# Kernel optimization log

Hardware: AMD Instinct MI355X
Metric: run time of the kernel (lower is better)

The kernel has to match this reference:

```python
import jax, jax.numpy as jnp
import numpy as np

D, H, K, L, F, G, M, OUT = 1280, 16, 80, 4, 5120, 48, 2, 2048
HALF = K // 2  # rotary half dim = 40


def _token_coords(grid_thw, merge_size, N):
    tpi = grid_thw[:, 0] * grid_thw[:, 1] * grid_thw[:, 2]
    cu = jnp.concatenate([jnp.zeros(1, jnp.int32), jnp.cumsum(tpi).astype(jnp.int32)])
    tok = jnp.arange(N, dtype=jnp.int32)
    img_id = jnp.searchsorted(cu[1:], tok, side='right')
    local = tok - cu[img_id]
    h = grid_thw[img_id, 1]
    w = grid_thw[img_id, 2]
    spatial = local % (h * w)
    msq = merge_size * merge_size
    mw = w // merge_size
    group, intra = spatial // msq, spatial % msq
    row = (group // mw) * merge_size + intra // merge_size
    col = (group % mw) * merge_size + intra % merge_size
    return row, col, h, w, cu


def _layernorm(x, s, b, eps=1e-6):
    mu = jnp.mean(x, -1, keepdims=True)
    var = jnp.mean(jnp.square(x - mu), -1, keepdims=True)
    return (x - mu) * jax.lax.rsqrt(var + eps) * s + b


def _rotate_half(x):
    x1, x2 = x[..., :HALF], x[..., HALF:]
    return jnp.concatenate([-x2, x1], axis=-1)


def setup_inputs() -> dict:
    key = jax.random.key(0)
    ks = jax.random.split(key, 16)
    s = 0.02
    inp = {
        'pixels': jax.random.normal(ks[0], (2048, 1536), jnp.float32),
        'grid_thw': jnp.array([[1, 16, 32]] * 4, jnp.int32),
        'pos_embed': jax.random.normal(ks[1], (G * G, D), jnp.float32) * s,
        'patch_w': jax.random.normal(ks[2], (1536, D), jnp.float32) * s,
        'patch_b': jnp.zeros((D,), jnp.float32),
        'ln1_s': jnp.ones((L, D), jnp.float32), 'ln1_b': jnp.zeros((L, D), jnp.float32),
        'qkv_w': jax.random.normal(ks[3], (L, D, 3 * D), jnp.float32) * s,
        'qkv_b': jnp.zeros((L, 3 * D), jnp.float32),
        'proj_w': jax.random.normal(ks[4], (L, D, D), jnp.float32) * s,
        'proj_b': jnp.zeros((L, D), jnp.float32),
        'ln2_s': jnp.ones((L, D), jnp.float32), 'ln2_b': jnp.zeros((L, D), jnp.float32),
        'fc1_w': jax.random.normal(ks[5], (L, D, F), jnp.float32) * s,
        'fc1_b': jnp.zeros((L, F), jnp.float32),
        'fc2_w': jax.random.normal(ks[6], (L, F, D), jnp.float32) * s,
        'fc2_b': jnp.zeros((L, D), jnp.float32),
        'm_norm_s': jnp.ones((D,), jnp.float32), 'm_norm_b': jnp.zeros((D,), jnp.float32),
        'm_fc1_w': jax.random.normal(ks[7], (D * M * M, D * M * M), jnp.float32) * s,
        'm_fc1_b': jnp.zeros((D * M * M,), jnp.float32),
        'm_fc2_w': jax.random.normal(ks[8], (D * M * M, OUT), jnp.float32) * s,
        'm_fc2_b': jnp.zeros((OUT,), jnp.float32),
    }
    return inp


def _forward(pixels, grid_thw, pos_embed, patch_w, patch_b, ln1_s, ln1_b, qkv_w, qkv_b,
             proj_w, proj_b, ln2_s, ln2_b, fc1_w, fc1_b, fc2_w, fc2_b,
             m_norm_s, m_norm_b, m_fc1_w, m_fc1_b, m_fc2_w, m_fc2_b):
    N = pixels.shape[0]
    row, col, h, w, cu = _token_coords(grid_thw, M, N)

    # patch embed: conv with stride==kernel over flattened patches == linear
    x = pixels @ patch_w + patch_b  # [N, D]

    # bilinear position-embedding interpolation onto each image's (h, w) grid
    rf = jnp.where(h > 1, row.astype(jnp.float32) * (G - 1) / jnp.maximum(h - 1, 1), 0.0)
    cf = jnp.where(w > 1, col.astype(jnp.float32) * (G - 1) / jnp.maximum(w - 1, 1), 0.0)
    r0 = jnp.floor(rf).astype(jnp.int32); r1 = jnp.minimum(r0 + 1, G - 1)
    c0 = jnp.floor(cf).astype(jnp.int32); c1 = jnp.minimum(c0 + 1, G - 1)
    wr = (rf - r0)[:, None]; wc = (cf - c0)[:, None]
    pe = (pos_embed[r0 * G + c0] * (1 - wr) * (1 - wc)
          + pos_embed[r0 * G + c1] * (1 - wr) * wc
          + pos_embed[r1 * G + c0] * wr * (1 - wc)
          + pos_embed[r1 * G + c1] * wr * wc)
    x = x + pe

    # 2-D rotary embeddings
    inv_freq = 1.0 / (10000.0 ** (jnp.arange(0, HALF, 2, dtype=jnp.float32) / HALF))
    freqs = jnp.concatenate([row[:, None].astype(jnp.float32) * inv_freq,
                             col[:, None].astype(jnp.float32) * inv_freq], axis=-1)  # [N, HALF]
    emb = jnp.concatenate([freqs, freqs], axis=-1)  # [N, K]
    cos, sin = jnp.cos(emb)[:, None, :], jnp.sin(emb)[:, None, :]  # [N,1,K]

    # block-diagonal segment mask via cu_seqlens (N is a multiple of 128; no pad)
    tok = jnp.arange(N)
    seg = jnp.searchsorted(cu[1:], tok, side='right')
    k_start = cu[jnp.minimum(seg, cu.shape[0] - 2)]
    k_end = cu[jnp.minimum(seg + 1, cu.shape[0] - 1)]
    mask = (tok[None, :] >= k_start[:, None]) & (tok[None, :] < k_end[:, None])  # [N,N]
    scale = K ** -0.5

    for l in range(L):
        hdn = _layernorm(x, ln1_s[l], ln1_b[l])
        qkv = (hdn @ qkv_w[l] + qkv_b[l]).reshape(N, 3, H, K)
        q, k, v = qkv[:, 0], qkv[:, 1], qkv[:, 2]
        q = q * cos + _rotate_half(q) * sin
        k = k * cos + _rotate_half(k) * sin
        scores = jnp.einsum('nhk,mhk->hnm', q, k) * scale
        scores = jnp.where(mask[None], scores, jnp.finfo(scores.dtype).min)
        attn = jax.nn.softmax(scores, axis=-1)
        o = jnp.einsum('hnm,mhk->nhk', attn, v).reshape(N, D)
        x = x + o @ proj_w[l] + proj_b[l]

        hdn = _layernorm(x, ln2_s[l], ln2_b[l])
        ff = jax.nn.gelu(hdn @ fc1_w[l] + fc1_b[l], approximate=True)
        x = x + ff @ fc2_w[l] + fc2_b[l]

    # patch merger
    normed = _layernorm(x, m_norm_s, m_norm_b).reshape(N // (M * M), D * M * M)
    ff = jax.nn.gelu(normed @ m_fc1_w + m_fc1_b, approximate=True)
    return ff @ m_fc2_w + m_fc2_b  # [N/4, OUT]


def reference(pixels, grid_thw, pos_embed, patch_w, patch_b, ln1_s, ln1_b, qkv_w, qkv_b,
              proj_w, proj_b, ln2_s, ln2_b, fc1_w, fc1_b, fc2_w, fc2_b,
              m_norm_s, m_norm_b, m_fc1_w, m_fc1_b, m_fc2_w, m_fc2_b):
    return _forward(pixels, grid_thw, pos_embed, patch_w, patch_b, ln1_s, ln1_b, qkv_w, qkv_b,
                    proj_w, proj_b, ln2_s, ln2_b, fc1_w, fc1_b, fc2_w, fc2_b,
                    m_norm_s, m_norm_b, m_fc1_w, m_fc1_b, m_fc2_w, m_fc2_b)
```

## Files before the change

### kernel.cpp

```cpp
#include <hip/hip_runtime.h>
#include <math.h>

#define DMODEL 1280
#define NHEADS 16
#define FDIM   5120
#define GPOS   48
#define SEG    512

typedef __attribute__((ext_vector_type(8))) short bf16x8;
typedef __attribute__((ext_vector_type(4))) float f32x4;
typedef unsigned short u16;

__device__ __forceinline__ u16 f2bf(float f) {
  unsigned int u = __float_as_uint(f);
  u = (u + 0x7FFFu + ((u >> 16) & 1u)) >> 16;
  return (u16)u;
}
__device__ __forceinline__ float bf2f(u16 u) {
  return __uint_as_float((unsigned int)u << 16);
}
__device__ __forceinline__ float gelu_tanh(float x) {
  float u = 0.7978845608028654f * (x + 0.044715f * x * x * x);
  float t = __expf(2.f * u);
  float th = 1.f - 2.f / (t + 1.f);
  return 0.5f * x * (1.f + th);
}

typedef const __attribute__((address_space(1))) unsigned int* gas_t;
typedef __attribute__((address_space(3))) unsigned int* las_t;
__device__ __forceinline__ void async16(const void* g, void* l) {
  __builtin_amdgcn_global_load_lds((gas_t)g, (las_t)l, 16, 0, 0);
}

__device__ __forceinline__ int xcd_remap(int b, int nwg) {
  int q = nwg >> 3, r = nwg & 7, x = b & 7, d = b >> 3;
  return (x < r ? x * (q + 1) : r * (q + 1) + (x - r) * q) + d;
}

#define STG256(mat, PW, ldx, h, kk, pp)                          \
  do {                                                           \
    const u16* g_ = (PW) + (long long)(h) * 128 * (ldx) + (kk);  \
    async16(g_, &L[pp][mat][h][(w * 2 + 0) * 512]);              \
    async16(g_ + 32, &L[pp][mat][h][(w * 2 + 1) * 512]);         \
  } while (0)

#define MM256(ii, ff)                                                          \
  acc[ii][ff] = __builtin_amdgcn_mfma_f32_16x16x32_bf16(aR[(ii) & 3][0],       \
                    bR[ff][0], acc[ii][ff], 0, 0, 0);                          \
  acc[ii][ff] = __builtin_amdgcn_mfma_f32_16x16x32_bf16(aR[(ii) & 3][1],       \
                    bR[ff][1], acc[ii][ff], 0, 0, 0);

#define BAR256() asm volatile("s_barrier" ::: "memory")
#define LGKM0() asm volatile("s_waitcnt lgkmcnt(0)" ::: "memory")

template <int EPI>
__global__ __launch_bounds__(512, 2) void gemm256(
    const u16* __restrict__ A, const u16* __restrict__ B,
    const float* __restrict__ bias, void* __restrict__ Cv,
    int Kd, int lda, int ldb, int ldc, int nsplit, long long pstride) {
  __shared__ __align__(16) u16 L[2][2][2][8192];
  const int sp = blockIdx.z;
  const int Ks = Kd / nsplit;
  const int NT = Ks >> 6;
  const u16* Ab = A + (long long)sp * Ks;
  const u16* Bb = B + (long long)sp * Ks;
  const int gx = gridDim.x;
  const int lg = xcd_remap(blockIdx.x + gx * blockIdx.y, gx * gridDim.y);
  const int m0 = (lg % gx) * 256, n0 = (lg / gx) * 256;
  const int t = threadIdx.x, ln = t & 63, w = t >> 6;
  const int wr = w >> 2, wc = w & 3;
  const int m16 = ln & 15, q = ln >> 4;
  const int r16 = ln >> 2;
  const int csw = (ln & 3) ^ ((ln >> 5) << 1);
  const int rbase = m16 * 32 + (q ^ ((m16 >> 3) << 1)) * 8;

  const u16* Aw = Ab + (long long)(m0 + w * 16 + r16) * lda + csw * 8;
  const u16* Bw = Bb + (long long)(n0 + w * 16 + r16) * ldb + csw * 8;

  f32x4 acc[8][4];
#pragma unroll
  for (int i = 0; i < 8; i++)
#pragma unroll
    for (int j = 0; j < 4; j++)
#pragma unroll
      for (int r = 0; r < 4; r++) acc[i][j][r] = 0.f;

  STG256(0, Aw, lda, 0, 0, 0);
  STG256(0, Aw, lda, 1, 0, 0);
  STG256(1, Bw, ldb, 0, 0, 0);
  STG256(1, Bw, ldb, 1, 0, 0);
  if (NT > 1) {
    STG256(1, Bw, ldb, 0, 64, 1);
    STG256(1, Bw, ldb, 1, 64, 1);
    asm volatile("s_waitcnt vmcnt(4)" ::: "memory");
  } else {
    asm volatile("s_waitcnt vmcnt(0)" ::: "memory");
  }
  BAR256();

  const int wb = (wc & 1) * 4;
  for (int tt = 0; tt < NT; ++tt) {
    const int p = tt & 1;
    const u16* Abuf = &L[p][0][wr][0];
    const u16* Bbuf = &L[p][1][wc >> 1][0];
    bf16x8 aR[4][2], bR[4][2];

#pragma unroll
    for (int i = 0; i < 4; ++i) {
      aR[i][0] = *(const bf16x8*)(Abuf + (i * 2 + 0) * 512 + rbase);
      aR[i][1] = *(const bf16x8*)(Abuf + (i * 2 + 1) * 512 + rbase);
    }
#pragma unroll
    for (int fc = 0; fc < 2; ++fc) {
      bR[fc][0] = *(const bf16x8*)(Bbuf + ((wb + fc) * 2 + 0) * 512 + rbase);
      bR[fc][1] = *(const bf16x8*)(Bbuf + ((wb + fc) * 2 + 1) * 512 + rbase);
    }
    if (tt + 1 < NT) STG256(0, Aw, lda, 0, (tt + 1) * 64, (tt + 1) & 1);
    BAR256();
    LGKM0();
    __builtin_amdgcn_s_setprio(1);
#pragma unroll
    for (int i = 0; i < 4; ++i) { MM256(i, 0); MM256(i, 1); }
    __builtin_amdgcn_s_setprio(0);
    BAR256();

#pragma unroll
    for (int fc = 2; fc < 4; ++fc) {
      bR[fc][0] = *(const bf16x8*)(Bbuf + ((wb + fc) * 2 + 0) * 512 + rbase);
      bR[fc][1] = *(const bf16x8*)(Bbuf + ((wb + fc) * 2 + 1) * 512 + rbase);
    }
    if (tt + 1 < NT) STG256(0, Aw, lda, 1, (tt + 1) * 64, (tt + 1) & 1);
    BAR256();
    LGKM0();
    __builtin_amdgcn_s_setprio(1);
#pragma unroll
    for (int i = 0; i < 4; ++i) { MM256(i, 2); MM256(i, 3); }
    __builtin_amdgcn_s_setprio(0);
    BAR256();

#pragma unroll
    for (int i = 0; i < 4; ++i) {
      aR[i][0] = *(const bf16x8*)(Abuf + ((4 + i) * 2 + 0) * 512 + rbase);
      aR[i][1] = *(const bf16x8*)(Abuf + ((4 + i) * 2 + 1) * 512 + rbase);
    }
    if (tt + 2 < NT) STG256(1, Bw, ldb, 0, (tt + 2) * 64, p);
    BAR256();
    LGKM0();
    __builtin_amdgcn_s_setprio(1);
#pragma unroll
    for (int i = 0; i < 4; ++i) { MM256(4 + i, 2); MM256(4 + i, 3); }
    __builtin_amdgcn_s_setprio(0);
    BAR256();

    if (tt + 2 < NT) STG256(1, Bw, ldb, 1, (tt + 2) * 64, p);
    BAR256();
    LGKM0();
    __builtin_amdgcn_s_setprio(1);
#pragma unroll
    for (int i = 0; i < 4; ++i) { MM256(4 + i, 0); MM256(4 + i, 1); }
    __builtin_amdgcn_s_setprio(0);
    if (tt + 1 < NT) {
      if (tt + 2 < NT) asm volatile("s_waitcnt vmcnt(4)" ::: "memory");
      else             asm volatile("s_waitcnt vmcnt(0)" ::: "memory");
    }
    BAR256();
  }

#pragma unroll
  for (int fr = 0; fr < 8; fr++) {
#pragma unroll
    for (int r = 0; r < 4; r++) {
      int row = m0 + wr * 128 + fr * 16 + q * 4 + r;
      if (EPI == 0) {
        u16* Cp = (u16*)Cv + (long long)sp * pstride + (long long)row * ldc;
#pragma unroll
        for (int fc = 0; fc < 4; fc++)
          Cp[n0 + wc * 64 + fc * 16 + m16] = f2bf(acc[fr][fc][r]);
      } else if (EPI == 1) {
        u16* Cb = (u16*)Cv + (long long)row * ldc;
#pragma unroll
        for (int fc = 0; fc < 4; fc++) {
          int col = n0 + wc * 64 + fc * 16 + m16;
          Cb[col] = f2bf(acc[fr][fc][r] + bias[col]);
        }
      } else {
        u16* Cb = (u16*)Cv + (long long)row * ldc;
#pragma unroll
        for (int fc = 0; fc < 4; fc++) {
          int col = n0 + wc * 64 + fc * 16 + m16;
          Cb[col] = f2bf(gelu_tanh(acc[fr][fc][r] + bias[col]));
        }
      }
    }
  }
}

__global__ __launch_bounds__(256) void fattn_k(
    const u16* __restrict__ qr, const u16* __restrict__ kr,
    const u16* __restrict__ vpT, u16* __restrict__ o, int N, float iscale) {
  __shared__ __align__(16) u16 Ks[2][24][512];
  __shared__ __align__(16) u16 Vs[2][20][512];
  __shared__ __align__(16) u16 Ps[4][32 * 128];
  const int nseg = N >> 9;
  const int gx = gridDim.x;
  const int lg = xcd_remap(blockIdx.x + gx * blockIdx.y, gx * gridDim.y);
  const int strip = lg % gx, hb = lg / gx;
  const int h = hb / nseg, seg = hb - h * nseg;
  const int t = threadIdx.x, ln = t & 63, w = t >> 6;
  const int m16 = ln & 15, qh = ln >> 4;
  const int r4 = ln >> 2, gsw = (ln & 3) ^ ((ln >> 5) << 1);
  const int rbase = m16 * 32 + ((qh ^ ((m16 >> 3) << 1)) << 3);
  const long long hN = (long long)h * N;
  const int segbase = seg * SEG;
  const int q0 = segbase + strip * 128 + w * 32;

  bf16x8 qf[2][3];
#pragma unroll
  for (int mi = 0; mi < 2; mi++)
#pragma unroll
    for (int ks = 0; ks < 3; ks++)
      qf[mi][ks] = *(const bf16x8*)&qr[(hN + q0 + mi * 16 + m16) * 96 + ks * 32 + qh * 8];

  f32x4 ao[2][5];
#pragma unroll
  for (int mi = 0; mi < 2; mi++)
#pragma unroll
    for (int df = 0; df < 5; df++)
#pragma unroll
      for (int r = 0; r < 4; r++) ao[mi][df][r] = 0.f;
  float m_[2][4], l_[2][4];
#pragma unroll
  for (int mi = 0; mi < 2; mi++)
#pragma unroll
    for (int r = 0; r < 4; r++) { m_[mi][r] = -1e30f; l_[mi][r] = 0.f; }

  auto stage = [&](int c, int pb) {
#pragma unroll
    for (int i = 0; i < 6; i++) {
      int sK = w * 6 + i, f = sK / 3, kg = sK - f * 3;
      async16(&kr[(hN + segbase + c * 128 + f * 16 + r4) * 96 + kg * 32 + gsw * 8],
              &Ks[pb][sK][0]);
    }
#pragma unroll
    for (int i = 0; i < 5; i++) {
      int sV = w * 5 + i, df = sV >> 2, kvg = sV & 3;
      async16(&vpT[((long long)hb * 128 + df * 16 + r4) * SEG + c * 128 + kvg * 32 + gsw * 8],
              &Vs[pb][sV][0]);
    }
  };

  stage(0, 0);
  u16* Pmy = &Ps[w][0];
  for (int c = 0; c < 4; c++) {
    const int pb = c & 1;
    __syncthreads();
    if (c < 3) stage(c + 1, pb ^ 1);

    f32x4 s[2][8];
#pragma unroll
    for (int mi = 0; mi < 2; mi++)
#pragma unroll
      for (int f = 0; f < 8; f++)
#pragma unroll
        for (int r = 0; r < 4; r++) s[mi][f][r] = 0.f;
#pragma unroll
    for (int ks = 0; ks < 3; ks++) {
#pragma unroll
      for (int f = 0; f < 8; f++) {
        bf16x8 kf = *(const bf16x8*)&Ks[pb][f * 3 + ks][rbase];
#pragma unroll
        for (int mi = 0; mi < 2; mi++)
          s[mi][f] = __builtin_amdgcn_mfma_f32_16x16x32_bf16(qf[mi][ks], kf, s[mi][f], 0, 0, 0);
      }
    }

#pragma unroll
    for (int mi = 0; mi < 2; mi++) {
#pragma unroll
      for (int r = 0; r < 4; r++) {
        float mx = s[mi][0][r];
#pragma unroll
        for (int f = 1; f < 8; f++) mx = fmaxf(mx, s[mi][f][r]);
        mx *= iscale;
#pragma unroll
        for (int o2 = 1; o2 <= 8; o2 <<= 1) mx = fmaxf(mx, __shfl_xor(mx, o2));
        float mn = fmaxf(m_[mi][r], mx);
        float corr = __expf(m_[mi][r] - mn);
        m_[mi][r] = mn;
        float rs = 0.f;
#pragma unroll
        for (int f = 0; f < 8; f++) {
          float p = __expf(s[mi][f][r] * iscale - mn);
          s[mi][f][r] = p;
          rs += p;
        }
#pragma unroll
        for (int o2 = 1; o2 <= 8; o2 <<= 1) rs += __shfl_xor(rs, o2);
        l_[mi][r] = l_[mi][r] * corr + rs;
#pragma unroll
        for (int df = 0; df < 5; df++) ao[mi][df][r] *= corr;
      }
    }

#pragma unroll
    for (int mi = 0; mi < 2; mi++) {
#pragma unroll
      for (int r = 0; r < 4; r++) {
        int qq = mi * 16 + qh * 4 + r;
        int base = qq * 128 + (m16 & 7);
        int ql = qq & 7;
#pragma unroll
        for (int f = 0; f < 8; f++) {
          int gr = (f * 2 + (m16 >> 3)) ^ ql;
          Pmy[base + gr * 8] = f2bf(s[mi][f][r]);
        }
      }
    }

#pragma unroll
    for (int ks = 0; ks < 4; ks++) {
      bf16x8 pf[2];
#pragma unroll
      for (int mi = 0; mi < 2; mi++)
        pf[mi] = *(const bf16x8*)&Pmy[(mi * 16 + m16) * 128 +
                                      (((ks * 4 + qh) ^ (m16 & 7)) << 3)];
#pragma unroll
      for (int df = 0; df < 5; df++) {
        bf16x8 vf = *(const bf16x8*)&Vs[pb][df * 4 + ks][rbase];
#pragma unroll
        for (int mi = 0; mi < 2; mi++)
          ao[mi][df] = __builtin_amdgcn_mfma_f32_16x16x32_bf16(pf[mi], vf, ao[mi][df], 0, 0, 0);
      }
    }
  }

#pragma unroll
  for (int mi = 0; mi < 2; mi++) {
#pragma unroll
    for (int r = 0; r < 4; r++) {
      float rl = 1.f / l_[mi][r];
      long long rowb = (long long)(q0 + mi * 16 + qh * 4 + r) * DMODEL + h * 80;
#pragma unroll
      for (int df = 0; df < 5; df++)
        o[rowb + df * 16 + m16] = f2bf(ao[mi][df][r] * rl);
    }
  }
}

template <int S, int RES, int GELU, int OUTBF>
__global__ void reduce_k(const u16* __restrict__ Pp, long long mn, int Nn,
                         const float* __restrict__ bias,
                         const float* __restrict__ res, void* __restrict__ out) {
  long long i = ((long long)blockIdx.x * 256 + threadIdx.x) * 4;
  if (i >= mn) return;
  float vx = 0.f, vy = 0.f, vz = 0.f, vw = 0.f;
#pragma unroll
  for (int s = 0; s < S; s++) {
    ushort4 u4 = *(const ushort4*)(Pp + (long long)s * mn + i);
    vx += bf2f(u4.x); vy += bf2f(u4.y); vz += bf2f(u4.z); vw += bf2f(u4.w);
  }
  int col = (int)(i % Nn);
  vx += bias[col]; vy += bias[col + 1]; vz += bias[col + 2]; vw += bias[col + 3];
  if (GELU) {
    vx = gelu_tanh(vx); vy = gelu_tanh(vy);
    vz = gelu_tanh(vz); vw = gelu_tanh(vw);
  }
  if (RES) {
    float4 r4 = *(const float4*)(res + i);
    vx += r4.x; vy += r4.y; vz += r4.z; vw += r4.w;
  }
  if (OUTBF) {
    ushort4 o; o.x = f2bf(vx); o.y = f2bf(vy); o.z = f2bf(vz); o.w = f2bf(vw);
    *(ushort4*)((u16*)out + i) = o;
  } else {
    float4 o; o.x = vx; o.y = vy; o.z = vz; o.w = vw;
    *(float4*)((float*)out + i) = o;
  }
}

template <int S>
__global__ void redln_k(const u16* __restrict__ Pp, long long mn,
                        const float* __restrict__ bias,
                        float* __restrict__ x,
                        const float* __restrict__ s, const float* __restrict__ b,
                        u16* __restrict__ h) {
  int row = blockIdx.x;
  int d = threadIdx.x * 4;
  long long base = (long long)row * DMODEL + d;
  float vx = 0.f, vy = 0.f, vz = 0.f, vw = 0.f;
#pragma unroll
  for (int si = 0; si < S; si++) {
    ushort4 u4 = *(const ushort4*)(Pp + (long long)si * mn + base);
    vx += bf2f(u4.x); vy += bf2f(u4.y); vz += bf2f(u4.z); vw += bf2f(u4.w);
  }
  vx += bias[d]; vy += bias[d + 1]; vz += bias[d + 2]; vw += bias[d + 3];
  float4 r4 = *(const float4*)(x + base);
  vx += r4.x; vy += r4.y; vz += r4.z; vw += r4.w;
  float4 xv; xv.x = vx; xv.y = vy; xv.z = vz; xv.w = vw;
  *(float4*)(x + base) = xv;
  float sum = vx + vy + vz + vw;
#pragma unroll
  for (int o = 32; o; o >>= 1) sum += __shfl_xor(sum, o);
  __shared__ float red[8];
  int wv = threadIdx.x >> 6, lnn = threadIdx.x & 63;
  if (lnn == 0) red[wv] = sum;
  __syncthreads();
  float mu = 0.f;
  for (int i = 0; i < 5; i++) mu += red[i];
  mu *= (1.f / DMODEL);
  float dx = vx - mu, dy = vy - mu, dz = vz - mu, dw = vw - mu;
  float s2 = dx * dx + dy * dy + dz * dz + dw * dw;
#pragma unroll
  for (int o = 32; o; o >>= 1) s2 += __shfl_xor(s2, o);
  __syncthreads();
  if (lnn == 0) red[wv] = s2;
  __syncthreads();
  float var = 0.f;
  for (int i = 0; i < 5; i++) var += red[i];
  var *= (1.f / DMODEL);
  float rs = rsqrtf(var + 1e-6f);
  ushort4 o4;
  o4.x = f2bf(dx * rs * s[d] + b[d]);
  o4.y = f2bf(dy * rs * s[d + 1] + b[d + 1]);
  o4.z = f2bf(dz * rs * s[d + 2] + b[d + 2]);
  o4.w = f2bf(dw * rs * s[d + 3] + b[d + 3]);
  *(ushort4*)(h + base) = o4;
}

__global__ void wconv_k(const float* __restrict__ in, u16* __restrict__ out,
                        int K, int N) {
  __shared__ float tl[32][33];
  int n0 = blockIdx.x * 32, k0 = blockIdx.y * 32;
  int t = threadIdx.x;
  int r = t >> 5, c = t & 31;
#pragma unroll
  for (int i = 0; i < 4; i++)
    tl[r + 8 * i][c] = in[(long long)(k0 + r + 8 * i) * N + n0 + c];
  __syncthreads();
  int n = t >> 4, kp = (t & 15) * 2;
#pragma unroll
  for (int i = 0; i < 2; i++) {
    ushort2 o;
    o.x = f2bf(tl[kp][n + 16 * i]);
    o.y = f2bf(tl[kp + 1][n + 16 * i]);
    *(ushort2*)&out[(long long)(n0 + n + 16 * i) * K + k0 + kp] = o;
  }
}

__global__ void conv_k(const float* __restrict__ in, u16* __restrict__ out,
                       long long n) {
  long long i = ((long long)blockIdx.x * 256 + threadIdx.x) * 4;
  if (i >= n) return;
  float4 v = *(const float4*)(in + i);
  ushort4 o; o.x = f2bf(v.x); o.y = f2bf(v.y); o.z = f2bf(v.z); o.w = f2bf(v.w);
  *(ushort4*)&out[i] = o;
}

union U16x8 { uint4 v; u16 s[8]; };
__global__ void vtr_k(const u16* __restrict__ in, u16* __restrict__ out) {
  __shared__ u16 tl[64][65];
  int b = blockIdx.z;
  int m0 = blockIdx.x * 64;
  int d0 = blockIdx.y * 64;
  const u16* ib = in + (long long)b * SEG * 128;
  u16* ob = out + (long long)b * 128 * SEG;
  int t = threadIdx.x;
  int r = t >> 3, c8 = (t & 7) * 8;
#pragma unroll
  for (int i = 0; i < 2; i++) {
    U16x8 ld;
    ld.v = *(const uint4*)&ib[(long long)(m0 + r + 32 * i) * 128 + d0 + c8];
#pragma unroll
    for (int j = 0; j < 8; j++) tl[r + 32 * i][c8 + j] = ld.s[j];
  }
  __syncthreads();
  int d = t >> 3, m8 = (t & 7) * 8;
#pragma unroll
  for (int i = 0; i < 2; i++) {
    int dd = d + 32 * i;
    U16x8 st;
#pragma unroll
    for (int j = 0; j < 8; j++) st.s[j] = tl[m8 + j][dd];
    *(uint4*)&ob[(long long)(d0 + dd) * SEG + m0 + m8] = st.v;
  }
}

__global__ void coords_k(const int* __restrict__ g, int nimg,
                         int* __restrict__ rw, int* __restrict__ cl,
                         int* __restrict__ hh, int* __restrict__ ww, int N) {
  int t = blockIdx.x * 256 + threadIdx.x;
  if (t >= N) return;
  int c = 0, local = 0, H = 1, W = 1;
  for (int i = 0; i < nimg; i++) {
    int tpi = g[i * 3] * g[i * 3 + 1] * g[i * 3 + 2];
    if (t >= c && t < c + tpi) { local = t - c; H = g[i * 3 + 1]; W = g[i * 3 + 2]; }
    c += tpi;
  }
  int hw = H * W;
  int sp = local % hw;
  int mw = W >> 1;
  int gr = sp >> 2, intra = sp & 3;
  rw[t] = (gr / mw) * 2 + (intra >> 1);
  cl[t] = (gr % mw) * 2 + (intra & 1);
  hh[t] = H; ww[t] = W;
}

__global__ void peadd_k(float* __restrict__ x, const float* __restrict__ pe,
                        const int* __restrict__ rw, const int* __restrict__ cl,
                        const int* __restrict__ hh, const int* __restrict__ ww) {
  int n = blockIdx.x;
  int d = threadIdx.x * 4;
  int H = hh[n], W = ww[n];
  float rf = (H > 1) ? (float)rw[n] * (float)(GPOS - 1) / (float)(H - 1) : 0.f;
  float cf = (W > 1) ? (float)cl[n] * (float)(GPOS - 1) / (float)(W - 1) : 0.f;
  int r0 = (int)floorf(rf), c0 = (int)floorf(cf);
  int r1 = min(r0 + 1, GPOS - 1), c1 = min(c0 + 1, GPOS - 1);
  float wr = rf - (float)r0, wc = cf - (float)c0;
  float w00 = (1.f - wr) * (1.f - wc), w01 = (1.f - wr) * wc;
  float w10 = wr * (1.f - wc), w11 = wr * wc;
  float4 v00 = *(const float4*)(pe + (long long)(r0 * GPOS + c0) * DMODEL + d);
  float4 v01 = *(const float4*)(pe + (long long)(r0 * GPOS + c1) * DMODEL + d);
  float4 v10 = *(const float4*)(pe + (long long)(r1 * GPOS + c0) * DMODEL + d);
  float4 v11 = *(const float4*)(pe + (long long)(r1 * GPOS + c1) * DMODEL + d);
  float4 xv = *(float4*)(x + (long long)n * DMODEL + d);
  xv.x += w00 * v00.x + w01 * v01.x + w10 * v10.x + w11 * v11.x;
  xv.y += w00 * v00.y + w01 * v01.y + w10 * v10.y + w11 * v11.y;
  xv.z += w00 * v00.z + w01 * v01.z + w10 * v10.z + w11 * v11.z;
  xv.w += w00 * v00.w + w01 * v01.w + w10 * v10.w + w11 * v11.w;
  *(float4*)(x + (long long)n * DMODEL + d) = xv;
}

__global__ void ln_k(const float* __restrict__ X, u16* __restrict__ Y,
                     const float* __restrict__ s, const float* __restrict__ b) {
  int row = blockIdx.x;
  int d = threadIdx.x * 4;
  const float* x = X + (long long)row * DMODEL;
  float4 v = *(const float4*)(x + d);
  float sum = v.x + v.y + v.z + v.w;
#pragma unroll
  for (int o = 32; o; o >>= 1) sum += __shfl_xor(sum, o);
  __shared__ float red[8];
  int wv = threadIdx.x >> 6, lnn = threadIdx.x & 63;
  if (lnn == 0) red[wv] = sum;
  __syncthreads();
  float mu = 0.f;
  for (int i = 0; i < 5; i++) mu += red[i];
  mu *= (1.f / DMODEL);
  float dx = v.x - mu, dy = v.y - mu, dz = v.z - mu, dw = v.w - mu;
  float s2 = dx * dx + dy * dy + dz * dz + dw * dw;
#pragma unroll
  for (int o = 32; o; o >>= 1) s2 += __shfl_xor(s2, o);
  __syncthreads();
  if (lnn == 0) red[wv] = s2;
  __syncthreads();
  float var = 0.f;
  for (int i = 0; i < 5; i++) var += red[i];
  var *= (1.f / DMODEL);
  float rs = rsqrtf(var + 1e-6f);
  ushort4 o4;
  o4.x = f2bf(dx * rs * s[d] + b[d]);
  o4.y = f2bf(dy * rs * s[d + 1] + b[d + 1]);
  o4.z = f2bf(dz * rs * s[d + 2] + b[d + 2]);
  o4.w = f2bf(dw * rs * s[d + 3] + b[d + 3]);
  *(ushort4*)(Y + (long long)row * DMODEL + d) = o4;
}

__global__ void rope_k(const u16* __restrict__ qkv, const int* __restrict__ rw,
                       const int* __restrict__ cl, u16* __restrict__ qr,
                       u16* __restrict__ kr, u16* __restrict__ vp, int N) {
  int n = blockIdx.x, h = blockIdx.y, t = threadIdx.x;
  const u16* src = qkv + (long long)n * (3 * DMODEL) + h * 80;
  long long ob96 = ((long long)h * N + n) * 96;
  long long ob128 = ((long long)h * N + n) * 128;
  if (t < 40) {
    float pos = (t < 20) ? (float)rw[n] : (float)cl[n];
    float infr = exp2f(-13.287712379549449f * (float)(t % 20) * 0.05f);
    float f = pos * infr;
    float cs = cosf(f), sn = sinf(f);
    float q0 = bf2f(src[t]), q1 = bf2f(src[t + 40]);
    qr[ob96 + t] = f2bf(q0 * cs - q1 * sn);
    qr[ob96 + t + 40] = f2bf(q1 * cs + q0 * sn);
    float k0 = bf2f(src[DMODEL + t]), k1 = bf2f(src[DMODEL + t + 40]);
    kr[ob96 + t] = f2bf(k0 * cs - k1 * sn);
    kr[ob96 + t + 40] = f2bf(k1 * cs + k0 * sn);
    vp[ob128 + t] = src[2 * DMODEL + t];
    vp[ob128 + t + 40] = src[2 * DMODEL + t + 40];
  } else {
    int u = t - 40;
    if (u < 16) { qr[ob96 + 80 + u] = 0; kr[ob96 + 80 + u] = 0; }
    vp[ob128 + 80 + u] = 0;
    vp[ob128 + 104 + u] = 0;
  }
}

static void gemm_big(hipStream_t st, int epi, const u16* A, const u16* B,
                     const float* bias, void* C, int M, int Nn, int Kd,
                     int lda, int ldb, int ldc, int nsplit) {
  dim3 g(M / 256, Nn / 256, nsplit), blk(512);
  long long ps = (long long)M * Nn;
  switch (epi) {
    case 0: gemm256<0><<<g, blk, 0, st>>>(A, B, bias, C, Kd, lda, ldb, ldc, nsplit, ps); break;
    case 1: gemm256<1><<<g, blk, 0, st>>>(A, B, bias, C, Kd, lda, ldb, ldc, nsplit, ps); break;
    default: gemm256<3><<<g, blk, 0, st>>>(A, B, bias, C, Kd, lda, ldb, ldc, nsplit, ps); break;
  }
}

extern "C" void kernel_launch(void* const* d_in, const int* in_sizes, int n_in,
                              void* d_out, int out_size, void* d_ws, size_t ws_size,
                              hipStream_t stream) {
  const float* pixels = (const float*)d_in[0];
  const int* grid_thw = (const int*)d_in[1];
  const float* pos_embed = (const float*)d_in[2];
  const float* patch_w = (const float*)d_in[3];
  const float* patch_b = (const float*)d_in[4];
  const float* ln1_s = (const float*)d_in[5];
  const float* ln1_b = (const float*)d_in[6];
  const float* qkv_w = (const float*)d_in[7];
  const float* qkv_b = (const float*)d_in[8];
  const float* proj_w = (const float*)d_in[9];
  const float* proj_b = (const float*)d_in[10];
  const float* ln2_s = (const float*)d_in[11];
  const float* ln2_b = (const float*)d_in[12];
  const float* fc1_w = (const float*)d_in[13];
  const float* fc1_b = (const float*)d_in[14];
  const float* fc2_w = (const float*)d_in[15];
  const float* fc2_b = (const float*)d_in[16];
  const float* mns = (const float*)d_in[17];
  const float* mnb = (const float*)d_in[18];
  const float* mf1w = (const float*)d_in[19];
  const float* mf1b = (const float*)d_in[20];
  const float* mf2w = (const float*)d_in[21];
  const float* mf2b = (const float*)d_in[22];
  float* out = (float*)d_out;

  const int N = in_sizes[0] / 1536;
  const int nimg = in_sizes[1] / 3;
  const int nseg = N / SEG;
  const int nb = NHEADS * nseg;

  char* w = (char*)d_ws;
  size_t off = 0;
  auto alloc = [&](size_t bytes) -> void* {
    void* p = w + off;
    off += (bytes + 255) & ~(size_t)255;
    return p;
  };
  int* rw = (int*)alloc((size_t)N * 4);
  int* cl = (int*)alloc((size_t)N * 4);
  int* hh = (int*)alloc((size_t)N * 4);
  int* ww = (int*)alloc((size_t)N * 4);
  float* x = (float*)alloc((size_t)N * DMODEL * 4);
  u16* h = (u16*)alloc((size_t)N * DMODEL * 2);
  u16* pixbf = (u16*)alloc((size_t)N * 1536 * 2);
  u16* patchT = (u16*)alloc((size_t)DMODEL * 1536 * 2);
  u16* qkvT = (u16*)alloc((size_t)3 * DMODEL * DMODEL * 2);
  u16* projT = (u16*)alloc((size_t)DMODEL * DMODEL * 2);
  u16* fc1T = (u16*)alloc((size_t)FDIM * DMODEL * 2);
  u16* fc2T = (u16*)alloc((size_t)DMODEL * FDIM * 2);
  u16* qkvb = (u16*)alloc((size_t)N * 3 * DMODEL * 2);
  u16* qr = (u16*)alloc((size_t)NHEADS * N * 96 * 2);
  u16* kr = (u16*)alloc((size_t)NHEADS * N * 96 * 2);
  u16* vp = (u16*)alloc((size_t)NHEADS * N * 128 * 2);
  u16* vpT = (u16*)alloc((size_t)NHEADS * N * 128 * 2);
  u16* pad0 = (u16*)alloc((size_t)nb * 2 * SEG * 128 * 2);
  u16* o = (u16*)alloc((size_t)N * DMODEL * 2);
  float* bigA = (float*)alloc((size_t)nb * SEG * SEG * 4);
  float* bigB = (float*)alloc((size_t)nb * SEG * SEG * 2);
  (void)ws_size; (void)pad0;
  u16* mfc1T = qkvb;
  u16* mfc2T = pixbf;
  u16* ffb = (u16*)bigA;
  u16* mf = (u16*)bigA;
  u16* part = (u16*)bigB;

  const float iscale = 0.11180339887498949f;
  const long long mnD = (long long)N * DMODEL;

  coords_k<<<dim3((N + 255) / 256), 256, 0, stream>>>(grid_thw, nimg, rw, cl, hh, ww, N);
  conv_k<<<dim3((int)(((long long)N * 1536 / 4 + 255) / 256)), 256, 0, stream>>>(
      pixels, pixbf, (long long)N * 1536);
  wconv_k<<<dim3(DMODEL / 32, 1536 / 32), 256, 0, stream>>>(patch_w, patchT, 1536, DMODEL);
  gemm_big(stream, 0, pixbf, patchT, nullptr, part, N, DMODEL, 1536, 1536, 1536,
           DMODEL, 4);
  reduce_k<4, 0, 0, 0><<<dim3((int)((mnD / 4 + 255) / 256)), 256, 0, stream>>>(
      part, mnD, DMODEL, patch_b, nullptr, x);
  peadd_k<<<dim3(N), 320, 0, stream>>>(x, pos_embed, rw, cl, hh, ww);
  ln_k<<<dim3(N), 320, 0, stream>>>(x, h, ln1_s, ln1_b);

  for (int l = 0; l < 4; l++) {
    wconv_k<<<dim3(3 * DMODEL / 32, DMODEL / 32), 256, 0, stream>>>(
        qkv_w + (size_t)l * DMODEL * 3 * DMODEL, qkvT, DMODEL, 3 * DMODEL);
    wconv_k<<<dim3(DMODEL / 32, DMODEL / 32), 256, 0, stream>>>(
        proj_w + (size_t)l * DMODEL * DMODEL, projT, DMODEL, DMODEL);
    wconv_k<<<dim3(FDIM / 32, DMODEL / 32), 256, 0, stream>>>(
        fc1_w + (size_t)l * DMODEL * FDIM, fc1T, DMODEL, FDIM);
    wconv_k<<<dim3(DMODEL / 32, FDIM / 32), 256, 0, stream>>>(
        fc2_w + (size_t)l * FDIM * DMODEL, fc2T, FDIM, DMODEL);

    gemm_big(stream, 1, h, qkvT, qkv_b + (size_t)l * 3 * DMODEL, qkvb, N,
             3 * DMODEL, DMODEL, DMODEL, DMODEL, 3 * DMODEL, 1);
    rope_k<<<dim3(N, NHEADS), 64, 0, stream>>>(qkvb, rw, cl, qr, kr, vp, N);
    vtr_k<<<dim3(8, 2, nb), 256, 0, stream>>>(vp, vpT);
    fattn_k<<<dim3(SEG / 128, nb), 256, 0, stream>>>(qr, kr, vpT, o, N, iscale);
    gemm_big(stream, 0, o, projT, nullptr, part, N, DMODEL, DMODEL, DMODEL,
             DMODEL, DMODEL, 4);
    redln_k<4><<<dim3(N), 320, 0, stream>>>(part, mnD, proj_b + (size_t)l * DMODEL,
                                            x, ln2_s + (size_t)l * DMODEL,
                                            ln2_b + (size_t)l * DMODEL, h);
    gemm_big(stream, 3, h, fc1T, fc1_b + (size_t)l * FDIM, ffb, N, FDIM, DMODEL,
             DMODEL, DMODEL, FDIM, 1);
    gemm_big(stream, 0, ffb, fc2T, nullptr, part, N, DMODEL, FDIM, FDIM, FDIM,
             DMODEL, 4);
    const float* nsl = (l < 3) ? ln1_s + (size_t)(l + 1) * DMODEL : mns;
    const float* nbl = (l < 3) ? ln1_b + (size_t)(l + 1) * DMODEL : mnb;
    redln_k<4><<<dim3(N), 320, 0, stream>>>(part, mnD, fc2_b + (size_t)l * DMODEL,
                                            x, nsl, nbl, h);
  }

  const int Mm = N / 4;
  wconv_k<<<dim3(FDIM / 32, FDIM / 32), 256, 0, stream>>>(mf1w, mfc1T, FDIM, FDIM);
  gemm_big(stream, 0, h, mfc1T, nullptr, part, Mm, FDIM, FDIM, FDIM, FDIM, FDIM, 4);
  reduce_k<4, 0, 1, 1><<<dim3((int)(((long long)Mm * FDIM / 4 + 255) / 256)), 256, 0, stream>>>(
      part, (long long)Mm * FDIM, FDIM, mf1b, nullptr, mf);
  wconv_k<<<dim3(2048 / 32, FDIM / 32), 256, 0, stream>>>(mf2w, mfc2T, FDIM, 2048);
  gemm_big(stream, 0, mf, mfc2T, nullptr, part, Mm, 2048, FDIM, FDIM, FDIM, 2048, 16);
  reduce_k<16, 0, 0, 0><<<dim3((int)(((long long)Mm * 2048 / 4 + 255) / 256)), 256, 0, stream>>>(
      part, (long long)Mm * 2048, 2048, mf2b, nullptr, out);
}
```

Baseline: 1.441 ms.

## Shrink big GEMM tile from 256x256 to 128x128 with 4-wave blocks

Replaces the 512-thread 256x256 GEMM kernel with a 256-thread 128x128 variant. The LDS staging, fragment loads and MFMA schedule are rewritten for a 2x2 wave layout with 4x4 accumulator tiles per wave. The aim is more workgroups for the small M (2048 tokens) so more CUs are busy. The cost is less data reuse per tile and more global traffic per FLOP. It also drops the LDS wait before the last two MFMA phases, which is fine only because those phases reuse fragments already in registers.

```diff
diff --git a/kernel.cpp b/kernel.cpp
--- a/kernel.cpp
+++ b/kernel.cpp
@@ -37,28 +37,25 @@
   return (x < r ? x * (q + 1) : r * (q + 1) + (x - r) * q) + d;
 }
 
-#define STG256(mat, PW, ldx, h, kk, pp)                          \
-  do {                                                           \
-    const u16* g_ = (PW) + (long long)(h) * 128 * (ldx) + (kk);  \
-    async16(g_, &L[pp][mat][h][(w * 2 + 0) * 512]);              \
-    async16(g_ + 32, &L[pp][mat][h][(w * 2 + 1) * 512]);         \
-  } while (0)
-
-#define MM256(ii, ff)                                                          \
-  acc[ii][ff] = __builtin_amdgcn_mfma_f32_16x16x32_bf16(aR[(ii) & 3][0],       \
-                    bR[ff][0], acc[ii][ff], 0, 0, 0);                          \
-  acc[ii][ff] = __builtin_amdgcn_mfma_f32_16x16x32_bf16(aR[(ii) & 3][1],       \
+#define STG1(mat, PW, ldx, rb, kh, kk, pp)                                  \
+  async16((PW) + (long long)(rb) * 16 * (ldx) + (kk) + (kh) * 32,           \
+          &L[pp][mat][((rb) * 2 + (kh)) * 512])
+
+#define MM1(ii, ff)                                                          \
+  acc[ii][ff] = __builtin_amdgcn_mfma_f32_16x16x32_bf16(aR[ii][0],           \
+                    bR[ff][0], acc[ii][ff], 0, 0, 0);                        \
+  acc[ii][ff] = __builtin_amdgcn_mfma_f32_16x16x32_bf16(aR[ii][1],           \
                     bR[ff][1], acc[ii][ff], 0, 0, 0);
 
-#define BAR256() asm volatile("s_barrier" ::: "memory")
+#define BARX() asm volatile("s_barrier" ::: "memory")
 #define LGKM0() asm volatile("s_waitcnt lgkmcnt(0)" ::: "memory")
 
 template <int EPI>
-__global__ __launch_bounds__(512, 2) void gemm256(
+__global__ __launch_bounds__(256, 2) void gemm128(
     const u16* __restrict__ A, const u16* __restrict__ B,
     const float* __restrict__ bias, void* __restrict__ Cv,
     int Kd, int lda, int ldb, int ldc, int nsplit, long long pstride) {
-  __shared__ __align__(16) u16 L[2][2][2][8192];
+  __shared__ __align__(16) u16 L[2][2][8192];
   const int sp = blockIdx.z;
   const int Ks = Kd / nsplit;
   const int NT = Ks >> 6;
@@ -66,111 +63,109 @@
   const u16* Bb = B + (long long)sp * Ks;
   const int gx = gridDim.x;
   const int lg = xcd_remap(blockIdx.x + gx * blockIdx.y, gx * gridDim.y);
-  const int m0 = (lg % gx) * 256, n0 = (lg / gx) * 256;
+  const int m0 = (lg % gx) * 128, n0 = (lg / gx) * 128;
   const int t = threadIdx.x, ln = t & 63, w = t >> 6;
-  const int wr = w >> 2, wc = w & 3;
+  const int wr = w >> 1, wc = w & 1;
   const int m16 = ln & 15, q = ln >> 4;
   const int r16 = ln >> 2;
   const int csw = (ln & 3) ^ ((ln >> 5) << 1);
   const int rbase = m16 * 32 + (q ^ ((m16 >> 3) << 1)) * 8;
 
-  const u16* Aw = Ab + (long long)(m0 + w * 16 + r16) * lda + csw * 8;
-  const u16* Bw = Bb + (long long)(n0 + w * 16 + r16) * ldb + csw * 8;
-
-  f32x4 acc[8][4];
-#pragma unroll
-  for (int i = 0; i < 8; i++)
+  const u16* Aw = Ab + (long long)(m0 + r16) * lda + csw * 8;
+  const u16* Bw = Bb + (long long)(n0 + r16) * ldb + csw * 8;
+  const int w4 = w + 4;
+
+  f32x4 acc[4][4];
+#pragma unroll
+  for (int i = 0; i < 4; i++)
 #pragma unroll
     for (int j = 0; j < 4; j++)
 #pragma unroll
       for (int r = 0; r < 4; r++) acc[i][j][r] = 0.f;
 
-  STG256(0, Aw, lda, 0, 0, 0);
-  STG256(0, Aw, lda, 1, 0, 0);
-  STG256(1, Bw, ldb, 0, 0, 0);
-  STG256(1, Bw, ldb, 1, 0, 0);
+  STG1(0, Aw, lda, w, 0, 0, 0);  STG1(0, Aw, lda, w, 1, 0, 0);
+  STG1(0, Aw, lda, w4, 0, 0, 0); STG1(0, Aw, lda, w4, 1, 0, 0);
+  STG1(1, Bw, ldb, w, 0, 0, 0);  STG1(1, Bw, ldb, w, 1, 0, 0);
+  STG1(1, Bw, ldb, w4, 0, 0, 0); STG1(1, Bw, ldb, w4, 1, 0, 0);
   if (NT > 1) {
-    STG256(1, Bw, ldb, 0, 64, 1);
-    STG256(1, Bw, ldb, 1, 64, 1);
+    STG1(1, Bw, ldb, w, 0, 64, 1);  STG1(1, Bw, ldb, w, 1, 64, 1);
+    STG1(1, Bw, ldb, w4, 0, 64, 1); STG1(1, Bw, ldb, w4, 1, 64, 1);
     asm volatile("s_waitcnt vmcnt(4)" ::: "memory");
   } else {
     asm volatile("s_waitcnt vmcnt(0)" ::: "memory");
   }
-  BAR256();
-
-  const int wb = (wc & 1) * 4;
+  BARX();
+
   for (int tt = 0; tt < NT; ++tt) {
     const int p = tt & 1;
-    const u16* Abuf = &L[p][0][wr][0];
-    const u16* Bbuf = &L[p][1][wc >> 1][0];
+    const u16* Abuf = &L[p][0][0];
+    const u16* Bbuf = &L[p][1][0];
     bf16x8 aR[4][2], bR[4][2];
 
 #pragma unroll
     for (int i = 0; i < 4; ++i) {
-      aR[i][0] = *(const bf16x8*)(Abuf + (i * 2 + 0) * 512 + rbase);
-      aR[i][1] = *(const bf16x8*)(Abuf + (i * 2 + 1) * 512 + rbase);
-    }
-#pragma unroll
-    for (int fc = 0; fc < 2; ++fc) {
-      bR[fc][0] = *(const bf16x8*)(Bbuf + ((wb + fc) * 2 + 0) * 512 + rbase);
-      bR[fc][1] = *(const bf16x8*)(Bbuf + ((wb + fc) * 2 + 1) * 512 + rbase);
-    }
-    if (tt + 1 < NT) STG256(0, Aw, lda, 0, (tt + 1) * 64, (tt + 1) & 1);
-    BAR256();
+      aR[i][0] = *(const bf16x8*)(Abuf + ((wr * 4 + i) * 2 + 0) * 512 + rbase);
+      aR[i][1] = *(const bf16x8*)(Abuf + ((wr * 4 + i) * 2 + 1) * 512 + rbase);
+    }
+    bR[0][0] = *(const bf16x8*)(Bbuf + ((wc * 4 + 0) * 2 + 0) * 512 + rbase);
+    bR[0][1] = *(const bf16x8*)(Bbuf + ((wc * 4 + 0) * 2 + 1) * 512 + rbase);
+    if (tt + 1 < NT) {
+      STG1(0, Aw, lda, w, 0, (tt + 1) * 64, p ^ 1);
+      STG1(0, Aw, lda, w, 1, (tt + 1) * 64, p ^ 1);
+    }
+    BARX();
     LGKM0();
     __builtin_amdgcn_s_setprio(1);
-#pragma unroll
-    for (int i = 0; i < 4; ++i) { MM256(i, 0); MM256(i, 1); }
+    MM1(0, 0); MM1(1, 0); MM1(2, 0); MM1(3, 0);
     __builtin_amdgcn_s_setprio(0);
-    BAR256();
-
-#pragma unroll
-    for (int fc = 2; fc < 4; ++fc) {
-      bR[fc][0] = *(const bf16x8*)(Bbuf + ((wb + fc) * 2 + 0) * 512 + rbase);
-      bR[fc][1] = *(const bf16x8*)(Bbuf + ((wb + fc) * 2 + 1) * 512 + rbase);
-    }
-    if (tt + 1 < NT) STG256(0, Aw, lda, 1, (tt + 1) * 64, (tt + 1) & 1);
-    BAR256();
+    BARX();
+
+#pragma unroll
+    for (int j = 1; j < 4; ++j) {
+      bR[j][0] = *(const bf16x8*)(Bbuf + ((wc * 4 + j) * 2 + 0) * 512 + rbase);
+      bR[j][1] = *(const bf16x8*)(Bbuf + ((wc * 4 + j) * 2 + 1) * 512 + rbase);
+    }
+    if (tt + 1 < NT) {
+      STG1(0, Aw, lda, w4, 0, (tt + 1) * 64, p ^ 1);
+      STG1(0, Aw, lda, w4, 1, (tt + 1) * 64, p ^ 1);
+    }
+    BARX();
     LGKM0();
     __builtin_amdgcn_s_setprio(1);
-#pragma unroll
-    for (int i = 0; i < 4; ++i) { MM256(i, 2); MM256(i, 3); }
+    MM1(0, 1); MM1(1, 1); MM1(2, 1); MM1(3, 1);
     __builtin_amdgcn_s_setprio(0);
-    BAR256();
-
-#pragma unroll
-    for (int i = 0; i < 4; ++i) {
-      aR[i][0] = *(const bf16x8*)(Abuf + ((4 + i) * 2 + 0) * 512 + rbase);
-      aR[i][1] = *(const bf16x8*)(Abuf + ((4 + i) * 2 + 1) * 512 + rbase);
-    }
-    if (tt + 2 < NT) STG256(1, Bw, ldb, 0, (tt + 2) * 64, p);
-    BAR256();
-    LGKM0();
+    BARX();
+
+    if (tt + 2 < NT) {
+      STG1(1, Bw, ldb, w, 0, (tt + 2) * 64, p);
+      STG1(1, Bw, ldb, w, 1, (tt + 2) * 64, p);
+    }
+    BARX();
     __builtin_amdgcn_s_setprio(1);
-#pragma unroll
-    for (int i = 0; i < 4; ++i) { MM256(4 + i, 2); MM256(4 + i, 3); }
+    MM1(0, 2); MM1(1, 2); MM1(2, 2); MM1(3, 2);
     __builtin_amdgcn_s_setprio(0);
-    BAR256();
-
-    if (tt + 2 < NT) STG256(1, Bw, ldb, 1, (tt + 2) * 64, p);
-    BAR256();
-    LGKM0();
+    BARX();
+
+    if (tt + 2 < NT) {
+      STG1(1, Bw, ldb, w4, 0, (tt + 2) * 64, p);
+      STG1(1, Bw, ldb, w4, 1, (tt + 2) * 64, p);
+    }
+    BARX();
     __builtin_amdgcn_s_setprio(1);
-#pragma unroll
-    for (int i = 0; i < 4; ++i) { MM256(4 + i, 0); MM256(4 + i, 1); }
+    MM1(0, 3); MM1(1, 3); MM1(2, 3); MM1(3, 3);
     __builtin_amdgcn_s_setprio(0);
     if (tt + 1 < NT) {
       if (tt + 2 < NT) asm volatile("s_waitcnt vmcnt(4)" ::: "memory");
       else             asm volatile("s_waitcnt vmcnt(0)" ::: "memory");
     }
-    BAR256();
-  }
-
-#pragma unroll
-  for (int fr = 0; fr < 8; fr++) {
+    BARX();
+  }
+
+#pragma unroll
+  for (int fr = 0; fr < 4; fr++) {
 #pragma unroll
     for (int r = 0; r < 4; r++) {
-      int row = m0 + wr * 128 + fr * 16 + q * 4 + r;
+      int row = m0 + wr * 64 + fr * 16 + q * 4 + r;
       if (EPI == 0) {
         u16* Cp = (u16*)Cv + (long long)sp * pstride + (long long)row * ldc;
 #pragma unroll
@@ -596,12 +591,12 @@
 static void gemm_big(hipStream_t st, int epi, const u16* A, const u16* B,
                      const float* bias, void* C, int M, int Nn, int Kd,
                      int lda, int ldb, int ldc, int nsplit) {
-  dim3 g(M / 256, Nn / 256, nsplit), blk(512);
+  dim3 g(M / 128, Nn / 128, nsplit), blk(256);
   long long ps = (long long)M * Nn;
   switch (epi) {
-    case 0: gemm256<0><<<g, blk, 0, st>>>(A, B, bias, C, Kd, lda, ldb, ldc, nsplit, ps); break;
-    case 1: gemm256<1><<<g, blk, 0, st>>>(A, B, bias, C, Kd, lda, ldb, ldc, nsplit, ps); break;
-    default: gemm256<3><<<g, blk, 0, st>>>(A, B, bias, C, Kd, lda, ldb, ldc, nsplit, ps); break;
+    case 0: gemm128<0><<<g, blk, 0, st>>>(A, B, bias, C, Kd, lda, ldb, ldc, nsplit, ps); break;
+    case 1: gemm128<1><<<g, blk, 0, st>>>(A, B, bias, C, Kd, lda, ldb, ldc, nsplit, ps); break;
+    default: gemm128<3><<<g, blk, 0, st>>>(A, B, bias, C, Kd, lda, ldb, ldc, nsplit, ps); break;
   }
 }
 
```

Result: faster. 1.366 ms (-5.2%).
